# Kernel tuning notes

Measured on AMD Instinct MI355X. Metric: run time of the kernel, lower is better.

Reference implementation:

```python
import jax, jax.numpy as jnp
import numpy as np

N = 102400      # total nodes (2048 molecules x 50 atoms)
E = 409600      # directed edges (avg degree 4)
B = 2048        # number of graphs in batch
F0 = 78         # num_features_mol
OUT = 200       # output_dim
MAXN = 64       # max_num nodes per graph (padding)


def _glorot(key, fan_in, fan_out):
    lim = jnp.sqrt(6.0 / (fan_in + fan_out)).astype(jnp.float32)
    return jax.random.uniform(key, (fan_in, fan_out), jnp.float32, -lim, lim)


def setup_inputs() -> dict:
    key = jax.random.key(0)
    ks = jax.random.split(key, 8)
    x = jax.random.normal(ks[0], (N, F0), jnp.float32)
    edge_index = jax.random.randint(ks[1], (2, E), 0, N, jnp.int32)
    # sorted contiguous graph assignment, 50 nodes per graph
    batch = jnp.repeat(jnp.arange(B, dtype=jnp.int32), N // B)
    return {
        "x": x,
        "edge_index": edge_index,
        "batch": batch,
        "max_num": MAXN,
        "W1": _glorot(ks[2], F0, F0),        "b1": jnp.zeros((F0,), jnp.float32),
        "W2": _glorot(ks[3], F0, 2 * F0),    "b2": jnp.zeros((2 * F0,), jnp.float32),
        "W3": _glorot(ks[4], 2 * F0, 4 * F0),"b3": jnp.zeros((4 * F0,), jnp.float32),
        "Wfc": _glorot(ks[5], 4 * F0, OUT),  "bfc": jnp.zeros((OUT,), jnp.float32),
    }


def _gcn_conv(h, W, b, src, dst, dinv):
    """PyG GCNConv: x' = D^{-1/2}(A+I)D^{-1/2} (x W) + b (with self-loops)."""
    h = h @ W                                  # [N, Fout]
    coef = (dinv[src] * dinv[dst])[:, None]    # [E, 1] symmetric norm
    agg = jax.ops.segment_sum(h[src] * coef, dst, num_segments=N)
    agg = agg + h * (dinv * dinv)[:, None]     # self-loop contribution (norm = 1/deg)
    return agg + b


def reference(x, edge_index, batch, max_num, W1, b1, W2, b2, W3, b3, Wfc, bfc):
    src, dst = edge_index[0], edge_index[1]
    # degree incl. self-loop, computed on destination nodes (PyG gcn_norm)
    deg = jax.ops.segment_sum(jnp.ones((E,), x.dtype), dst, num_segments=N) + 1.0
    dinv = jax.lax.rsqrt(deg)

    h = jax.nn.relu(_gcn_conv(x, W1, b1, src, dst, dinv))
    h = jax.nn.relu(_gcn_conv(h, W2, b2, src, dst, dinv))
    h = jax.nn.relu(_gcn_conv(h, W3, b3, src, dst, dinv))
    h = h @ Wfc + bfc                          # [N, OUT]

    # to_dense_batch: scatter each node into [B, max_num, OUT], truncating
    # nodes beyond max_num per graph (PyG semantics).
    counts = jax.ops.segment_sum(jnp.ones((N,), jnp.int32), batch, num_segments=B)
    starts = jnp.concatenate([jnp.zeros((1,), jnp.int32), jnp.cumsum(counts)[:-1]])
    pos = jnp.arange(N, dtype=jnp.int32) - starts[batch]   # index within graph
    valid = pos < max_num
    flat = jnp.where(valid, batch * max_num + pos, B * max_num)  # dropped -> dummy slot
    dense = jnp.zeros((B * max_num + 1, h.shape[1]), h.dtype).at[flat].set(h)
    return dense[:-1].reshape(B, max_num, h.shape[1])
```

## Files before the change

### kernel.cpp

```cpp
#include <hip/hip_runtime.h>
#include <hip/hip_bf16.h>
#include <stdint.h>

#define N_NODES 102400
#define N_EDGES 409600
#define N_GRAPHS 2048
#define MAXN 64
#define NPG 50
#define SLOT 32

typedef __attribute__((ext_vector_type(8))) short short8;
typedef __attribute__((ext_vector_type(4))) float f32x4;

static __device__ __forceinline__ float bfu2f(unsigned short u) {
    union { unsigned int i; float f; } v;
    v.i = ((unsigned int)u) << 16;
    return v.f;
}
static __device__ __forceinline__ unsigned short f2bfu(float f) {
    __hip_bfloat16 h = __float2bfloat16(f);
    return *reinterpret_cast<unsigned short*>(&h);
}


static __device__ __forceinline__ void prep_one(int i, const float* __restrict__ W,
                                                const float* __restrict__ b,
                                                int K, int Nc, int Kp, int Na,
                                                __hip_bfloat16* __restrict__ WT,
                                                float* __restrict__ bp) {
    int total = Na * Kp;
    if (i < total) {
        int c = i / Kp, k = i - c * Kp;
        float v = (c < Nc && k < K) ? W[k * Nc + c] : 0.0f;
        WT[i] = __float2bfloat16(v);
    }
    if (i < Na) bp[i] = (i < Nc) ? b[i] : 0.0f;
}

#define S1 (N_NODES * 48)
#define S2 (S1 + 180224)
#define S3 (S2 + N_EDGES)
#define S4 (S3 + N_GRAPHS * (MAXN - NPG) * 100)

__global__ void prologue_kernel(
    const float* __restrict__ X, __hip_bfloat16* __restrict__ xb,
    const float* __restrict__ W1, const float* __restrict__ b1,
    const float* __restrict__ W2, const float* __restrict__ b2,
    const float* __restrict__ W3, const float* __restrict__ b3,
    const float* __restrict__ Wf, const float* __restrict__ bf,
    __hip_bfloat16* __restrict__ WT1, float* __restrict__ b1p,
    __hip_bfloat16* __restrict__ WT2, float* __restrict__ b2p,
    __hip_bfloat16* __restrict__ WT3, float* __restrict__ b3p,
    __hip_bfloat16* __restrict__ WTF, float* __restrict__ bFp,
    const int* __restrict__ dst, int* __restrict__ deg,
    float* __restrict__ out) {
    int idx = blockIdx.x * blockDim.x + threadIdx.x;
    if (idx < S1) {
        int node = idx / 48;
        int c = idx - node * 48;
        int col = c * 2;
        float2 v = {0.0f, 0.0f};
        if (col < 78) v = *(const float2*)(X + (size_t)node * 78 + col);
        __hip_bfloat162 r;
        r.x = __float2bfloat16(v.x);
        r.y = __float2bfloat16(v.y);
        *(__hip_bfloat162*)(xb + (size_t)node * 96 + col) = r;
        return;
    }
    if (idx < S2) {
        int i = idx - S1;
        if (i < 12288) prep_one(i, W1, b1, 78, 78, 96, 128, WT1, b1p);
        else if (i < 36864) prep_one(i - 12288, W2, b2, 78, 156, 96, 256, WT2, b2p);
        else if (i < 98304) prep_one(i - 36864, W3, b3, 156, 312, 160, 384, WT3, b3p);
        else prep_one(i - 98304, Wf, bf, 312, 200, 320, 256, WTF, bFp);
        return;
    }
    if (idx < S3) {
        int e = idx - S2;
        atomicAdd(&deg[dst[e]], 1);
        return;
    }
    if (idx < S4) {
        int i = idx - S3;
        int b = i / ((MAXN - NPG) * 100);
        int u = i - b * ((MAXN - NPG) * 100);
        float2 z = {0.0f, 0.0f};
        *(float2*)(out + ((size_t)b * MAXN + NPG) * 200 + u * 2) = z;
    }
}

__global__ void dinv_kernel(const int* __restrict__ deg, float* __restrict__ dinv) {
    int i = blockIdx.x * blockDim.x + threadIdx.x;
    if (i < N_NODES) dinv[i] = rsqrtf((float)deg[i] + 1.0f);
}

__global__ void fill_kernel(const int* __restrict__ src, const int* __restrict__ dst,
                            int* __restrict__ cursor, int2* __restrict__ csr_pk,
                            const float* __restrict__ dinv) {
    int e = blockIdx.x * blockDim.x + threadIdx.x;
    if (e >= N_EDGES) return;
    int s = src[e], d = dst[e];
    int pos = atomicAdd(&cursor[d], 1);
    if (pos < SLOT) {
        float w = dinv[s] * dinv[d];
        int2 pk;
        pk.x = s;
        pk.y = __float_as_int(w);
        csr_pk[(size_t)d * SLOT + pos] = pk;
    }
}


template <int LD>
__global__ __launch_bounds__(256) void agg_bf16_w32(
    const __hip_bfloat16* __restrict__ H,
    const int* __restrict__ deg, const int2* __restrict__ csr_pk,
    const float* __restrict__ dinv,
    __hip_bfloat16* __restrict__ out) {
    constexpr int C = LD / 16;
    int idx = blockIdx.x * blockDim.x + threadIdx.x;
    if (idx >= N_NODES * C) return;
    int node = idx / C;
    int c = idx - node * C;
    const unsigned short* Hu = (const unsigned short*)H;
    size_t rowoff = (size_t)node * LD + c * 16;
    float di = dinv[node];
    float sw = di * di;
    short8 ha = *(const short8*)(Hu + rowoff);
    short8 hb = *(const short8*)(Hu + rowoff + 8);
    float a[16];
#pragma unroll
    for (int i = 0; i < 8; ++i) a[i] = sw * bfu2f((unsigned short)ha[i]);
#pragma unroll
    for (int i = 0; i < 8; ++i) a[8 + i] = sw * bfu2f((unsigned short)hb[i]);
    int e0 = node * SLOT, e1 = e0 + deg[node];
    int j = e0;
    for (; j + 2 <= e1; j += 2) {
        int2 p0 = csr_pk[j], p1 = csr_pk[j + 1];
        float w0 = __int_as_float(p0.y), w1 = __int_as_float(p1.y);
        const unsigned short* q0 = Hu + (size_t)p0.x * LD + c * 16;
        const unsigned short* q1 = Hu + (size_t)p1.x * LD + c * 16;
        short8 v0a = *(const short8*)(q0);
        short8 v0b = *(const short8*)(q0 + 8);
        short8 v1a = *(const short8*)(q1);
        short8 v1b = *(const short8*)(q1 + 8);
#pragma unroll
        for (int i = 0; i < 8; ++i) {
            a[i] += w0 * bfu2f((unsigned short)v0a[i]) + w1 * bfu2f((unsigned short)v1a[i]);
            a[8 + i] += w0 * bfu2f((unsigned short)v0b[i]) + w1 * bfu2f((unsigned short)v1b[i]);
        }
    }
    for (; j < e1; ++j) {
        int2 pk = csr_pk[j];
        float w = __int_as_float(pk.y);
        const unsigned short* qp = Hu + (size_t)pk.x * LD + c * 16;
        short8 va = *(const short8*)(qp);
        short8 vb = *(const short8*)(qp + 8);
#pragma unroll
        for (int i = 0; i < 8; ++i) {
            a[i] += w * bfu2f((unsigned short)va[i]);
            a[8 + i] += w * bfu2f((unsigned short)vb[i]);
        }
    }
    short8 ra, rb;
#pragma unroll
    for (int i = 0; i < 8; ++i) {
        ra[i] = (short)f2bfu(a[i]);
        rb[i] = (short)f2bfu(a[8 + i]);
    }
    *(short8*)((unsigned short*)out + rowoff) = ra;
    *(short8*)((unsigned short*)out + rowoff + 8) = rb;
}


template <int FOUT>
__global__ __launch_bounds__(256) void agg_gemm_kernel(
    const __hip_bfloat16* __restrict__ H,
    const int* __restrict__ deg, const int2* __restrict__ csr_pk,
    const float* __restrict__ dinv,
    const __hip_bfloat16* __restrict__ WT,
    const float* __restrict__ biasp,
    __hip_bfloat16* __restrict__ OutH) {
    constexpr int LDH = 96;
    constexpr int NB = FOUT / 32;
    constexpr int STRIDE = 208;
    constexpr int OSTR = FOUT * 2 + 16;
    __shared__ __align__(16) char aggT[128 * STRIDE];
    const int tid = threadIdx.x;
    const int r0 = blockIdx.x * 128;

    {
        const int row = tid >> 1;
        const int cb = (tid & 1) * 6;
        const int node = r0 + row;
        const unsigned short* Hu = (const unsigned short*)H;
        const unsigned short* selfp = Hu + (size_t)node * LDH + cb * 8;
        float di = dinv[node];
        float sw = di * di;
        float a[6][8];
        {
            short8 s[6];
#pragma unroll
            for (int q = 0; q < 6; ++q) s[q] = *(const short8*)(selfp + q * 8);
#pragma unroll
            for (int q = 0; q < 6; ++q)
#pragma unroll
                for (int i = 0; i < 8; ++i) a[q][i] = sw * bfu2f((unsigned short)s[q][i]);
        }
        int e0 = node * SLOT, e1 = e0 + deg[node];
        int j = e0;
        for (; j + 2 <= e1; j += 2) {
            int2 p0 = csr_pk[j], p1 = csr_pk[j + 1];
            float w0 = __int_as_float(p0.y), w1 = __int_as_float(p1.y);
            const unsigned short* q0 = Hu + (size_t)p0.x * LDH + cb * 8;
            const unsigned short* q1 = Hu + (size_t)p1.x * LDH + cb * 8;
            short8 v0[6], v1[6];
#pragma unroll
            for (int q = 0; q < 6; ++q) v0[q] = *(const short8*)(q0 + q * 8);
#pragma unroll
            for (int q = 0; q < 6; ++q) v1[q] = *(const short8*)(q1 + q * 8);
#pragma unroll
            for (int q = 0; q < 6; ++q)
#pragma unroll
                for (int i = 0; i < 8; ++i)
                    a[q][i] += w0 * bfu2f((unsigned short)v0[q][i]) +
                               w1 * bfu2f((unsigned short)v1[q][i]);
        }
        for (; j < e1; ++j) {
            int2 pk = csr_pk[j];
            float w = __int_as_float(pk.y);
            const unsigned short* qp = Hu + (size_t)pk.x * LDH + cb * 8;
            short8 v[6];
#pragma unroll
            for (int q = 0; q < 6; ++q) v[q] = *(const short8*)(qp + q * 8);
#pragma unroll
            for (int q = 0; q < 6; ++q)
#pragma unroll
                for (int i = 0; i < 8; ++i) a[q][i] += w * bfu2f((unsigned short)v[q][i]);
        }
        char* dstrow = aggT + row * STRIDE + cb * 16;
#pragma unroll
        for (int q = 0; q < 6; ++q) {
            short8 r;
#pragma unroll
            for (int i = 0; i < 8; ++i) r[i] = (short)f2bfu(a[q][i]);
            *(short8*)(dstrow + q * 16) = r;
        }
    }
    __syncthreads();

    const int lane = tid & 63;
    const int wid = tid >> 6;
    const int wr = wid >> 1, wc = wid & 1;
    const int frow = lane & 15;
    const int kq = lane >> 4;
    f32x4 acc[4][NB];
    {
        const __hip_bfloat16* bb[NB];
#pragma unroll
        for (int n = 0; n < NB; ++n)
            bb[n] = WT + (size_t)(wc * (FOUT / 2) + n * 16 + frow) * LDH + kq * 8;
        int abase[4];
#pragma unroll
        for (int m = 0; m < 4; ++m)
            abase[m] = (wr * 64 + m * 16 + frow) * STRIDE + kq * 16;
#pragma unroll
        for (int m = 0; m < 4; ++m)
#pragma unroll
            for (int n = 0; n < NB; ++n) {
                f32x4 z = {0.0f, 0.0f, 0.0f, 0.0f};
                acc[m][n] = z;
            }
#pragma unroll
        for (int t = 0; t < 3; ++t) {
            short8 af[4], bfr[NB];
#pragma unroll
            for (int m = 0; m < 4; ++m) af[m] = *(const short8*)(aggT + abase[m] + t * 64);
#pragma unroll
            for (int n = 0; n < NB; ++n) bfr[n] = *(const short8*)(bb[n] + t * 32);
#pragma unroll
            for (int m = 0; m < 4; ++m)
#pragma unroll
                for (int n = 0; n < NB; ++n)
                    acc[m][n] = __builtin_amdgcn_mfma_f32_16x16x32_bf16(bfr[n], af[m],
                                                                        acc[m][n], 0, 0, 0);
        }
    }

    float4 bv[NB];
#pragma unroll
    for (int n = 0; n < NB; ++n)
        bv[n] = *(const float4*)(biasp + (wc * (FOUT / 2) + n * 16 + (kq << 2)));
    constexpr int UNITS = FOUT / 8;
    constexpr int TOTAL = 64 * UNITS;
#pragma unroll
    for (int half = 0; half < 2; ++half) {
        __syncthreads();
        if (wr == half) {
#pragma unroll
            for (int m = 0; m < 4; ++m) {
                int srow = m * 16 + frow;
#pragma unroll
                for (int n = 0; n < NB; ++n) {
                    int col0 = wc * (FOUT / 2) + n * 16 + (kq << 2);
                    ushort4 o;
                    o.x = f2bfu(fmaxf(acc[m][n][0] + bv[n].x, 0.0f));
                    o.y = f2bfu(fmaxf(acc[m][n][1] + bv[n].y, 0.0f));
                    o.z = f2bfu(fmaxf(acc[m][n][2] + bv[n].z, 0.0f));
                    o.w = f2bfu(fmaxf(acc[m][n][3] + bv[n].w, 0.0f));
                    *(ushort4*)(aggT + srow * OSTR + col0 * 2) = o;
                }
            }
        }
        __syncthreads();
        for (int idx = tid; idx < TOTAL; idx += 256) {
            int r = idx / UNITS, u = idx - r * UNITS;
            int row = r0 + half * 64 + r;
            *(int4*)((unsigned short*)OutH + (size_t)row * FOUT + u * 8) =
                *(const int4*)(aggT + r * OSTR + u * 16);
        }
    }
}


__global__ __launch_bounds__(256) void gemm3fc_kernel(
    const __hip_bfloat16* __restrict__ A,
    const __hip_bfloat16* __restrict__ W3T,
    const float* __restrict__ b3p,
    const __hip_bfloat16* __restrict__ WTF,
    const float* __restrict__ bFp,
    float* __restrict__ out) {
    __shared__ __align__(16) char h3[64 * 640];
    const int tid = threadIdx.x;
    const int lane = tid & 63;
    const int w = tid >> 6;
    const int r0 = blockIdx.x * 64;
    const int frow = lane & 15;
    const int kq = lane >> 4;

    {
        const int row = tid >> 2;
        const int qb = (tid & 3) * 5;
        const __hip_bfloat16* ap = A + (size_t)(r0 + row) * 160 + qb * 8;
        char* dst = h3 + row * 336 + qb * 16;
        int4 v[5];
#pragma unroll
        for (int q = 0; q < 5; ++q) v[q] = *(const int4*)(ap + q * 8);
#pragma unroll
        for (int q = 0; q < 5; ++q) *(int4*)(dst + q * 16) = v[q];
    }

    const __hip_bfloat16* bb1[5];
#pragma unroll
    for (int n = 0; n < 5; ++n)
        bb1[n] = W3T + (size_t)(w * 80 + n * 16 + frow) * 160 + kq * 8;
    short8 bw[2][5];
#pragma unroll
    for (int n = 0; n < 5; ++n) bw[0][n] = *(const short8*)(bb1[n]);
#pragma unroll
    for (int n = 0; n < 5; ++n) bw[1][n] = *(const short8*)(bb1[n] + 32);

    __syncthreads();

    f32x4 acc1[4][5];
    {
        int abase1[4];
#pragma unroll
        for (int m = 0; m < 4; ++m) abase1[m] = (m * 16 + frow) * 336 + kq * 16;
#pragma unroll
        for (int m = 0; m < 4; ++m)
#pragma unroll
            for (int n = 0; n < 5; ++n) {
                f32x4 z = {0.0f, 0.0f, 0.0f, 0.0f};
                acc1[m][n] = z;
            }
#pragma unroll
        for (int t = 0; t < 5; ++t) {
            short8 af[4];
#pragma unroll
            for (int m = 0; m < 4; ++m) af[m] = *(const short8*)(h3 + abase1[m] + t * 64);
#pragma unroll
            for (int m = 0; m < 4; ++m)
#pragma unroll
                for (int n = 0; n < 5; ++n)
                    acc1[m][n] = __builtin_amdgcn_mfma_f32_16x16x32_bf16(bw[t & 1][n], af[m],
                                                                         acc1[m][n], 0, 0, 0);
            if (t + 2 < 5) {
#pragma unroll
                for (int n = 0; n < 5; ++n)
                    bw[t & 1][n] = *(const short8*)(bb1[n] + (t + 2) * 32);
            }
        }
    }
    __syncthreads();

#pragma unroll
    for (int m = 0; m < 4; ++m) {
        int row = m * 16 + frow;
        int swz = (row & 7) << 4;
#pragma unroll
        for (int n = 0; n < 5; ++n) {
            int col0 = w * 80 + n * 16 + (kq << 2);
            float4 bv = *(const float4*)(b3p + col0);
            ushort4 o;
            o.x = f2bfu(fmaxf(acc1[m][n][0] + bv.x, 0.0f));
            o.y = f2bfu(fmaxf(acc1[m][n][1] + bv.y, 0.0f));
            o.z = f2bfu(fmaxf(acc1[m][n][2] + bv.z, 0.0f));
            o.w = f2bfu(fmaxf(acc1[m][n][3] + bv.w, 0.0f));
            int byte = row * 640 + col0 * 2;
            *(ushort4*)(h3 + (byte ^ swz)) = o;
        }
    }

    const __hip_bfloat16* bb2[4];
#pragma unroll
    for (int n = 0; n < 4; ++n)
        bb2[n] = WTF + (size_t)(w * 64 + n * 16 + frow) * 320 + kq * 8;
    short8 bfr2[2][4];
#pragma unroll
    for (int n = 0; n < 4; ++n) bfr2[0][n] = *(const short8*)(bb2[n]);
#pragma unroll
    for (int n = 0; n < 4; ++n) bfr2[1][n] = *(const short8*)(bb2[n] + 32);

    __syncthreads();

    f32x4 acc[4][4];
    {
        int abase[4], aswz[4];
#pragma unroll
        for (int m = 0; m < 4; ++m) {
            int row = m * 16 + frow;
            abase[m] = row * 640 + kq * 16;
            aswz[m] = (row & 7) << 4;
        }
#pragma unroll
        for (int m = 0; m < 4; ++m)
#pragma unroll
            for (int n = 0; n < 4; ++n) {
                f32x4 z = {0.0f, 0.0f, 0.0f, 0.0f};
                acc[m][n] = z;
            }
#pragma unroll
        for (int t = 0; t < 10; ++t) {
            short8 af[4];
#pragma unroll
            for (int m = 0; m < 4; ++m)
                af[m] = *(const short8*)(h3 + ((abase[m] + t * 64) ^ aswz[m]));
#pragma unroll
            for (int m = 0; m < 4; ++m)
#pragma unroll
                for (int n = 0; n < 4; ++n)
                    acc[m][n] = __builtin_amdgcn_mfma_f32_16x16x32_bf16(bfr2[t & 1][n], af[m],
                                                                        acc[m][n], 0, 0, 0);
            if (t + 2 < 10) {
#pragma unroll
                for (int n = 0; n < 4; ++n)
                    bfr2[t & 1][n] = *(const short8*)(bb2[n] + (t + 2) * 32);
            }
        }
    }

    float4 bvF[4];
#pragma unroll
    for (int n = 0; n < 4; ++n)
        bvF[n] = *(const float4*)(bFp + (w * 64 + n * 16 + (kq << 2)));
#pragma unroll
    for (int half = 0; half < 2; ++half) {
        __syncthreads();
#pragma unroll
        for (int mm = 0; mm < 2; ++mm) {
            int m = half * 2 + mm;
            int srow = mm * 16 + frow;
#pragma unroll
            for (int n = 0; n < 4; ++n) {
                int col0 = w * 64 + n * 16 + (kq << 2);
                if (col0 >= 200) continue;
                float4 o;
                o.x = acc[m][n][0] + bvF[n].x;
                o.y = acc[m][n][1] + bvF[n].y;
                o.z = acc[m][n][2] + bvF[n].z;
                o.w = acc[m][n][3] + bvF[n].w;
                *(float4*)(h3 + srow * 816 + col0 * 4) = o;
            }
        }
        __syncthreads();
        for (int idx = tid; idx < 1600; idx += 256) {
            int r = idx / 50, f4 = idx - r * 50;
            int row = r0 + half * 32 + r;
            int drow = (row / NPG) * MAXN + (row % NPG);
            *(float4*)(out + (size_t)drow * 200 + f4 * 4) =
                *(const float4*)(h3 + r * 816 + f4 * 16);
        }
    }
}


static inline char* align256(char* p) {
    return (char*)(((uintptr_t)p + 255) & ~(uintptr_t)255);
}

extern "C" void kernel_launch(void* const* d_in, const int* in_sizes, int n_in,
                              void* d_out, int out_size, void* d_ws, size_t ws_size,
                              hipStream_t stream) {
    const int N = N_NODES, E = N_EDGES;
    const float* x = (const float*)d_in[0];
    const int* ei = (const int*)d_in[1];
    const int* src = ei;
    const int* dst = ei + E;
    const float* W1 = (const float*)d_in[4];
    const float* b1 = (const float*)d_in[5];
    const float* W2 = (const float*)d_in[6];
    const float* b2 = (const float*)d_in[7];
    const float* W3 = (const float*)d_in[8];
    const float* b3 = (const float*)d_in[9];
    const float* Wfc = (const float*)d_in[10];
    const float* bfc = (const float*)d_in[11];
    float* out = (float*)d_out;

    char* p = (char*)d_ws;
    int* deg = (int*)p;               p += (size_t)N * 4;
    int* cursor = (int*)p;            p = align256(p + (size_t)N * 4);
    float* dinv = (float*)p;          p = align256(p + (size_t)N * 4);
    int2* csr_pk = (int2*)p;          p = align256(p + (size_t)N * SLOT * 8);
    __hip_bfloat16* WT1 = (__hip_bfloat16*)p;  p = align256(p + 128 * 96 * 2);
    float* b1p = (float*)p;           p = align256(p + 128 * 4);
    __hip_bfloat16* WT2 = (__hip_bfloat16*)p;  p = align256(p + 256 * 96 * 2);
    float* b2p = (float*)p;           p = align256(p + 256 * 4);
    __hip_bfloat16* WT3 = (__hip_bfloat16*)p;  p = align256(p + 384 * 160 * 2);
    float* b3p = (float*)p;           p = align256(p + 384 * 4);
    __hip_bfloat16* WTF = (__hip_bfloat16*)p;  p = align256(p + 256 * 320 * 2);
    float* bFp = (float*)p;           p = align256(p + 256 * 4);
    __hip_bfloat16* bufAgg = (__hip_bfloat16*)p;  p = align256(p + (size_t)N * 320 * 2);
    __hip_bfloat16* bufH = (__hip_bfloat16*)p;    p = align256(p + (size_t)N * 320 * 2);

    hipMemsetAsync(deg, 0, (size_t)N * 8, stream);
    prologue_kernel<<<(S4 + 255) / 256, 256, 0, stream>>>(
        x, bufH, W1, b1, W2, b2, W3, b3, Wfc, bfc,
        WT1, b1p, WT2, b2p, WT3, b3p, WTF, bFp, dst, deg, out);
    dinv_kernel<<<(N + 255) / 256, 256, 0, stream>>>(deg, dinv);
    fill_kernel<<<(E + 255) / 256, 256, 0, stream>>>(src, dst, cursor, csr_pk, dinv);

    agg_gemm_kernel<96><<<N / 128, 256, 0, stream>>>(
        bufH, deg, csr_pk, dinv, WT1, b1p, bufAgg);

    agg_gemm_kernel<160><<<N / 128, 256, 0, stream>>>(
        bufAgg, deg, csr_pk, dinv, WT2, b2p, bufH);

    agg_bf16_w32<160><<<(N * 10 + 255) / 256, 256, 0, stream>>>(bufH, deg, csr_pk, dinv, bufAgg);
    gemm3fc_kernel<<<N / 64, 256, 0, stream>>>(bufAgg, WT3, b3p, WTF, bFp, out);
}
```

Before: 230.5 us.

## Fuse layer-3 aggregation into gemm3fc and drop the dinv kernel

The third-layer neighbor aggregation is moved into the prologue of gemm3fc_kernel, so aggregated rows go straight into shared memory and are never written to or read back from global memory. The separate dinv kernel is removed: edge weights are computed in fill_kernel as rsqrt of the product of degrees, and self-weights as 1/(deg+1). This saves two launches and one full intermediate buffer round trip. In exchange, each gemm3fc block does irregular gather work with fewer threads per row (4 threads over 160 columns), which may hurt latency hiding compared with the wider standalone aggregation kernel.

Measured after the change: 221.1 us. 4.1% less time.

```diff
diff --git a/kernel.cpp b/kernel.cpp
--- a/kernel.cpp
+++ b/kernel.cpp
@@ -89,20 +89,15 @@
     }
 }
 
-__global__ void dinv_kernel(const int* __restrict__ deg, float* __restrict__ dinv) {
-    int i = blockIdx.x * blockDim.x + threadIdx.x;
-    if (i < N_NODES) dinv[i] = rsqrtf((float)deg[i] + 1.0f);
-}
-
 __global__ void fill_kernel(const int* __restrict__ src, const int* __restrict__ dst,
                             int* __restrict__ cursor, int2* __restrict__ csr_pk,
-                            const float* __restrict__ dinv) {
+                            const int* __restrict__ deg) {
     int e = blockIdx.x * blockDim.x + threadIdx.x;
     if (e >= N_EDGES) return;
     int s = src[e], d = dst[e];
     int pos = atomicAdd(&cursor[d], 1);
     if (pos < SLOT) {
-        float w = dinv[s] * dinv[d];
+        float w = rsqrtf((float)(deg[s] + 1) * (float)(deg[d] + 1));
         int2 pk;
         pk.x = s;
         pk.y = __float_as_int(w);
@@ -111,73 +106,10 @@
 }
 
 
-template <int LD>
-__global__ __launch_bounds__(256) void agg_bf16_w32(
-    const __hip_bfloat16* __restrict__ H,
-    const int* __restrict__ deg, const int2* __restrict__ csr_pk,
-    const float* __restrict__ dinv,
-    __hip_bfloat16* __restrict__ out) {
-    constexpr int C = LD / 16;
-    int idx = blockIdx.x * blockDim.x + threadIdx.x;
-    if (idx >= N_NODES * C) return;
-    int node = idx / C;
-    int c = idx - node * C;
-    const unsigned short* Hu = (const unsigned short*)H;
-    size_t rowoff = (size_t)node * LD + c * 16;
-    float di = dinv[node];
-    float sw = di * di;
-    short8 ha = *(const short8*)(Hu + rowoff);
-    short8 hb = *(const short8*)(Hu + rowoff + 8);
-    float a[16];
-#pragma unroll
-    for (int i = 0; i < 8; ++i) a[i] = sw * bfu2f((unsigned short)ha[i]);
-#pragma unroll
-    for (int i = 0; i < 8; ++i) a[8 + i] = sw * bfu2f((unsigned short)hb[i]);
-    int e0 = node * SLOT, e1 = e0 + deg[node];
-    int j = e0;
-    for (; j + 2 <= e1; j += 2) {
-        int2 p0 = csr_pk[j], p1 = csr_pk[j + 1];
-        float w0 = __int_as_float(p0.y), w1 = __int_as_float(p1.y);
-        const unsigned short* q0 = Hu + (size_t)p0.x * LD + c * 16;
-        const unsigned short* q1 = Hu + (size_t)p1.x * LD + c * 16;
-        short8 v0a = *(const short8*)(q0);
-        short8 v0b = *(const short8*)(q0 + 8);
-        short8 v1a = *(const short8*)(q1);
-        short8 v1b = *(const short8*)(q1 + 8);
-#pragma unroll
-        for (int i = 0; i < 8; ++i) {
-            a[i] += w0 * bfu2f((unsigned short)v0a[i]) + w1 * bfu2f((unsigned short)v1a[i]);
-            a[8 + i] += w0 * bfu2f((unsigned short)v0b[i]) + w1 * bfu2f((unsigned short)v1b[i]);
-        }
-    }
-    for (; j < e1; ++j) {
-        int2 pk = csr_pk[j];
-        float w = __int_as_float(pk.y);
-        const unsigned short* qp = Hu + (size_t)pk.x * LD + c * 16;
-        short8 va = *(const short8*)(qp);
-        short8 vb = *(const short8*)(qp + 8);
-#pragma unroll
-        for (int i = 0; i < 8; ++i) {
-            a[i] += w * bfu2f((unsigned short)va[i]);
-            a[8 + i] += w * bfu2f((unsigned short)vb[i]);
-        }
-    }
-    short8 ra, rb;
-#pragma unroll
-    for (int i = 0; i < 8; ++i) {
-        ra[i] = (short)f2bfu(a[i]);
-        rb[i] = (short)f2bfu(a[8 + i]);
-    }
-    *(short8*)((unsigned short*)out + rowoff) = ra;
-    *(short8*)((unsigned short*)out + rowoff + 8) = rb;
-}
-
-
 template <int FOUT>
 __global__ __launch_bounds__(256) void agg_gemm_kernel(
     const __hip_bfloat16* __restrict__ H,
     const int* __restrict__ deg, const int2* __restrict__ csr_pk,
-    const float* __restrict__ dinv,
     const __hip_bfloat16* __restrict__ WT,
     const float* __restrict__ biasp,
     __hip_bfloat16* __restrict__ OutH) {
@@ -195,8 +127,8 @@
         const int node = r0 + row;
         const unsigned short* Hu = (const unsigned short*)H;
         const unsigned short* selfp = Hu + (size_t)node * LDH + cb * 8;
-        float di = dinv[node];
-        float sw = di * di;
+        int dg = deg[node];
+        float sw = 1.0f / (float)(dg + 1);
         float a[6][8];
         {
             short8 s[6];
@@ -207,7 +139,7 @@
 #pragma unroll
                 for (int i = 0; i < 8; ++i) a[q][i] = sw * bfu2f((unsigned short)s[q][i]);
         }
-        int e0 = node * SLOT, e1 = e0 + deg[node];
+        int e0 = node * SLOT, e1 = e0 + dg;
         int j = e0;
         for (; j + 2 <= e1; j += 2) {
             int2 p0 = csr_pk[j], p1 = csr_pk[j + 1];
@@ -324,7 +256,8 @@
 
 
 __global__ __launch_bounds__(256) void gemm3fc_kernel(
-    const __hip_bfloat16* __restrict__ A,
+    const __hip_bfloat16* __restrict__ H,
+    const int* __restrict__ deg, const int2* __restrict__ csr_pk,
     const __hip_bfloat16* __restrict__ W3T,
     const float* __restrict__ b3p,
     const __hip_bfloat16* __restrict__ WTF,
@@ -341,13 +274,60 @@
     {
         const int row = tid >> 2;
         const int qb = (tid & 3) * 5;
-        const __hip_bfloat16* ap = A + (size_t)(r0 + row) * 160 + qb * 8;
+        const int node = r0 + row;
+        const unsigned short* Hu = (const unsigned short*)H;
+        const unsigned short* selfp = Hu + (size_t)node * 160 + qb * 8;
+        int dg = deg[node];
+        float sw = 1.0f / (float)(dg + 1);
+        float a[5][8];
+        {
+            short8 s[5];
+#pragma unroll
+            for (int q = 0; q < 5; ++q) s[q] = *(const short8*)(selfp + q * 8);
+#pragma unroll
+            for (int q = 0; q < 5; ++q)
+#pragma unroll
+                for (int i = 0; i < 8; ++i) a[q][i] = sw * bfu2f((unsigned short)s[q][i]);
+        }
+        int e0 = node * SLOT, e1 = e0 + dg;
+        int j = e0;
+        for (; j + 2 <= e1; j += 2) {
+            int2 p0 = csr_pk[j], p1 = csr_pk[j + 1];
+            float w0 = __int_as_float(p0.y), w1 = __int_as_float(p1.y);
+            const unsigned short* q0 = Hu + (size_t)p0.x * 160 + qb * 8;
+            const unsigned short* q1 = Hu + (size_t)p1.x * 160 + qb * 8;
+            short8 v0[5], v1[5];
+#pragma unroll
+            for (int q = 0; q < 5; ++q) v0[q] = *(const short8*)(q0 + q * 8);
+#pragma unroll
+            for (int q = 0; q < 5; ++q) v1[q] = *(const short8*)(q1 + q * 8);
+#pragma unroll
+            for (int q = 0; q < 5; ++q)
+#pragma unroll
+                for (int i = 0; i < 8; ++i)
+                    a[q][i] += w0 * bfu2f((unsigned short)v0[q][i]) +
+                               w1 * bfu2f((unsigned short)v1[q][i]);
+        }
+        for (; j < e1; ++j) {
+            int2 pk = csr_pk[j];
+            float ww = __int_as_float(pk.y);
+            const unsigned short* qp = Hu + (size_t)pk.x * 160 + qb * 8;
+            short8 v[5];
+#pragma unroll
+            for (int q = 0; q < 5; ++q) v[q] = *(const short8*)(qp + q * 8);
+#pragma unroll
+            for (int q = 0; q < 5; ++q)
+#pragma unroll
+                for (int i = 0; i < 8; ++i) a[q][i] += ww * bfu2f((unsigned short)v[q][i]);
+        }
         char* dst = h3 + row * 336 + qb * 16;
-        int4 v[5];
-#pragma unroll
-        for (int q = 0; q < 5; ++q) v[q] = *(const int4*)(ap + q * 8);
-#pragma unroll
-        for (int q = 0; q < 5; ++q) *(int4*)(dst + q * 16) = v[q];
+#pragma unroll
+        for (int q = 0; q < 5; ++q) {
+            short8 r;
+#pragma unroll
+            for (int i = 0; i < 8; ++i) r[i] = (short)f2bfu(a[q][i]);
+            *(short8*)(dst + q * 16) = r;
+        }
     }
 
     const __hip_bfloat16* bb1[5];
@@ -520,7 +500,6 @@
     char* p = (char*)d_ws;
     int* deg = (int*)p;               p += (size_t)N * 4;
     int* cursor = (int*)p;            p = align256(p + (size_t)N * 4);
-    float* dinv = (float*)p;          p = align256(p + (size_t)N * 4);
     int2* csr_pk = (int2*)p;          p = align256(p + (size_t)N * SLOT * 8);
     __hip_bfloat16* WT1 = (__hip_bfloat16*)p;  p = align256(p + 128 * 96 * 2);
     float* b1p = (float*)p;           p = align256(p + 128 * 4);
@@ -537,15 +516,14 @@
     prologue_kernel<<<(S4 + 255) / 256, 256, 0, stream>>>(
         x, bufH, W1, b1, W2, b2, W3, b3, Wfc, bfc,
         WT1, b1p, WT2, b2p, WT3, b3p, WTF, bFp, dst, deg, out);
-    dinv_kernel<<<(N + 255) / 256, 256, 0, stream>>>(deg, dinv);
-    fill_kernel<<<(E + 255) / 256, 256, 0, stream>>>(src, dst, cursor, csr_pk, dinv);
+    fill_kernel<<<(E + 255) / 256, 256, 0, stream>>>(src, dst, cursor, csr_pk, deg);
 
     agg_gemm_kernel<96><<<N / 128, 256, 0, stream>>>(
-        bufH, deg, csr_pk, dinv, WT1, b1p, bufAgg);
+        bufH, deg, csr_pk, WT1, b1p, bufAgg);
 
     agg_gemm_kernel<160><<<N / 128, 256, 0, stream>>>(
-        bufAgg, deg, csr_pk, dinv, WT2, b2p, bufH);
-
-    agg_bf16_w32<160><<<(N * 10 + 255) / 256, 256, 0, stream>>>(bufH, deg, csr_pk, dinv, bufAgg);
-    gemm3fc_kernel<<<N / 64, 256, 0, stream>>>(bufAgg, WT3, b3p, WTF, bFp, out);
-}
+        bufAgg, deg, csr_pk, WT2, b2p, bufH);
+
+    gemm3fc_kernel<<<N / 64, 256, 0, stream>>>(
+        bufH, deg, csr_pk, WT3, b3p, WTF, bFp, out);
+}
```
